# Kernel optimization log

Hardware: AMD Instinct MI355X
Metric: run time of the kernel (lower is better)

The kernel has to match this reference:

```python
import jax, jax.numpy as jnp
import numpy as np


def setup_inputs() -> dict:
    key = jax.random.key(0)
    ks = jax.random.split(key, 5)
    T, H, I, E = 8192, 2048, 1408, 16
    return {
        "x": jax.random.normal(ks[0], (T, H), dtype=jnp.float32),
        "gate_w": jax.random.normal(ks[1], (E, H), dtype=jnp.float32) * 0.02,
        "W1": jax.random.normal(ks[2], (E, I, H), dtype=jnp.float32) * 0.02,
        "Up": jax.random.normal(ks[3], (E, I, H), dtype=jnp.float32) * 0.02,
        "W2": jax.random.normal(ks[4], (E, H, I), dtype=jnp.float32) * 0.02,
        "topk": 2,
    }


def reference(x, gate_w, W1, Up, W2, topk):
    # x: [T, H]; gate_w: [E, H]; W1/Up: [E, I, H]; W2: [E, H, I]
    E = gate_w.shape[0]
    logits = x @ gate_w.T                                   # [T, E]
    topk_w, topk_ids = jax.lax.top_k(logits, topk)          # [T, K]
    topk_w = jax.nn.softmax(topk_w, axis=-1)                # softmax over selected experts
    # combine weight per (token, expert): sum of routing weights where expert selected
    cw = jnp.sum(jax.nn.one_hot(topk_ids, E, dtype=x.dtype) * topk_w[..., None], axis=1)  # [T, E]

    def body(acc, inputs):
        w1, up, w2, we = inputs                             # [I,H],[I,H],[H,I],[T]
        h = jax.nn.silu(x @ w1.T) * (x @ up.T)              # [T, I]
        return acc + we[:, None] * (h @ w2.T), None

    out, _ = jax.lax.scan(body, jnp.zeros_like(x), (W1, Up, W2, cw.T))
    return out
```

## Files before the change

kernel.cpp:

```cpp
#include <hip/hip_runtime.h>

static constexpr int kT = 8192;
static constexpr int kH = 2048;
static constexpr int kI = 1408;
static constexpr int kE = 16;

typedef __bf16 bf16x8 __attribute__((ext_vector_type(8)));
typedef float floatx4 __attribute__((ext_vector_type(4)));

__device__ __forceinline__ __bf16 f2bf(float f) { return (__bf16)f; }

__global__ void cvt_x_kernel(const float* __restrict__ x, __bf16* __restrict__ xb) {
    size_t i = ((size_t)blockIdx.x * 256 + threadIdx.x) * 8;
    float4 v0 = *(const float4*)(x + i);
    float4 v1 = *(const float4*)(x + i + 4);
    union { __bf16 b[8]; uint4 u; } o;
    o.b[0] = f2bf(v0.x); o.b[1] = f2bf(v0.y); o.b[2] = f2bf(v0.z); o.b[3] = f2bf(v0.w);
    o.b[4] = f2bf(v1.x); o.b[5] = f2bf(v1.y); o.b[6] = f2bf(v1.z); o.b[7] = f2bf(v1.w);
    *(uint4*)(xb + i) = o.u;
}

__global__ __launch_bounds__(256)
void gate_kernel(const float* __restrict__ x, const float* __restrict__ gw,
                 int* __restrict__ t_ids, float* __restrict__ t_w,
                 int* __restrict__ counts) {
    const int lane = threadIdx.x & 63;
    const int t = blockIdx.x * 4 + (threadIdx.x >> 6);
    float acc[kE];
#pragma unroll
    for (int e = 0; e < kE; ++e) acc[e] = 0.f;
    const float* xr = x + (size_t)t * kH;
    for (int h = lane; h < kH; h += 64) {
        const float xv = xr[h];
#pragma unroll
        for (int e = 0; e < kE; ++e) acc[e] += xv * gw[e * kH + h];
    }
#pragma unroll
    for (int e = 0; e < kE; ++e) {
        float v = acc[e];
        for (int off = 32; off > 0; off >>= 1) v += __shfl_xor(v, off, 64);
        acc[e] = v;
    }
    if (lane == 0) {
        int i0 = 0; float l0 = acc[0];
#pragma unroll
        for (int e = 1; e < kE; ++e) if (acc[e] > l0) { l0 = acc[e]; i0 = e; }
        int i1 = -1; float l1 = -3.4e38f;
#pragma unroll
        for (int e = 0; e < kE; ++e) if (e != i0 && acc[e] > l1) { l1 = acc[e]; i1 = e; }
        const float ex = __expf(l1 - l0);
        const float inv = 1.f / (1.f + ex);
        t_ids[2 * t] = i0; t_ids[2 * t + 1] = i1;
        t_w[2 * t] = inv;  t_w[2 * t + 1] = ex * inv;
        atomicAdd(counts + i0, 1);
        atomicAdd(counts + i1, 1);
    }
}

__global__ void scan_kernel(const int* __restrict__ counts, int* __restrict__ offs,
                            int* __restrict__ fill) {
    if (threadIdx.x == 0) {
        int s = 0;
        for (int e = 0; e < kE; ++e) { offs[e] = s; fill[e] = s; s += counts[e]; }
        offs[kE] = s;
    }
}

__global__ void scatter_kernel(const int* __restrict__ t_ids, const float* __restrict__ t_w,
                               int* __restrict__ fill, int* __restrict__ btok,
                               float* __restrict__ bw) {
    int t = blockIdx.x * 256 + threadIdx.x;
    if (t < kT) {
#pragma unroll
        for (int k = 0; k < 2; ++k) {
            int e = t_ids[2 * t + k];
            int pos = atomicAdd(fill + e, 1);
            btok[pos] = t;
            bw[pos] = t_w[2 * t + k];
        }
    }
}

__global__ __launch_bounds__(256, 2)
void gemm1_kernel(const __bf16* __restrict__ xb, const float* __restrict__ W1,
                  const float* __restrict__ Up, const int* __restrict__ btok,
                  const float* __restrict__ bw, const int* __restrict__ offs,
                  __bf16* __restrict__ hbuf) {
    const int e = blockIdx.z;
    const int seg0 = offs[e];
    const int ne = offs[e + 1] - seg0;
    const int m0 = blockIdx.y * 128;
    if (m0 >= ne) return;
    const int n0 = blockIdx.x * 64;

    __shared__ __align__(16) __bf16 sA[128 * 64];
    __shared__ __align__(16) __bf16 sB1[64 * 64];
    __shared__ __align__(16) __bf16 sB2[64 * 64];

    const int tid = threadIdx.x;

    const int ar = tid >> 3;
    const int ac = (tid & 7) * 8;
    const __bf16* aptr[4];
#pragma unroll
    for (int i = 0; i < 4; ++i) {
        int rr = m0 + ar + 32 * i;
        if (rr >= ne) rr = ne - 1;
        aptr[i] = xb + (size_t)btok[seg0 + rr] * kH + ac;
    }

    const int brr = tid >> 4;
    const int bcc = (tid & 15) * 4;
    const float* b1p = W1 + ((size_t)e * kI + n0 + brr) * kH + bcc;
    const float* b2p = Up + ((size_t)e * kI + n0 + brr) * kH + bcc;

    const int wid = tid >> 6, lane = tid & 63;
    const int wm = (wid >> 1) * 64, wn = (wid & 1) * 32;
    const int lr = lane & 15;
    const int lk = (lane >> 4) * 8;

    floatx4 acc1[4][2], acc2[4][2];
#pragma unroll
    for (int i = 0; i < 4; ++i)
#pragma unroll
        for (int j = 0; j < 2; ++j) { acc1[i][j] = (floatx4)0.f; acc2[i][j] = (floatx4)0.f; }

    for (int k0 = 0; k0 < kH; k0 += 64) {
        __syncthreads();
#pragma unroll
        for (int i = 0; i < 4; ++i) {
            uint4 v = *(const uint4*)(aptr[i] + k0);
            *(uint4*)(sA + (ar + 32 * i) * 64 + ac) = v;
        }
#pragma unroll
        for (int i = 0; i < 4; ++i) {
            float4 v1 = *(const float4*)(b1p + (size_t)(16 * i) * kH + k0);
            float4 v2 = *(const float4*)(b2p + (size_t)(16 * i) * kH + k0);
            union { __bf16 b[4]; uint2 u; } o1, o2;
            o1.b[0] = f2bf(v1.x); o1.b[1] = f2bf(v1.y); o1.b[2] = f2bf(v1.z); o1.b[3] = f2bf(v1.w);
            o2.b[0] = f2bf(v2.x); o2.b[1] = f2bf(v2.y); o2.b[2] = f2bf(v2.z); o2.b[3] = f2bf(v2.w);
            *(uint2*)(sB1 + (brr + 16 * i) * 64 + bcc) = o1.u;
            *(uint2*)(sB2 + (brr + 16 * i) * 64 + bcc) = o2.u;
        }
        __syncthreads();
#pragma unroll
        for (int ks = 0; ks < 2; ++ks) {
            const int kk = ks * 32 + lk;
            bf16x8 af[4], bf1[2], bf2[2];
#pragma unroll
            for (int i = 0; i < 4; ++i)
                af[i] = *(const bf16x8*)(sA + (wm + i * 16 + lr) * 64 + kk);
#pragma unroll
            for (int j = 0; j < 2; ++j) {
                bf1[j] = *(const bf16x8*)(sB1 + (wn + j * 16 + lr) * 64 + kk);
                bf2[j] = *(const bf16x8*)(sB2 + (wn + j * 16 + lr) * 64 + kk);
            }
#pragma unroll
            for (int i = 0; i < 4; ++i)
#pragma unroll
                for (int j = 0; j < 2; ++j) {
                    acc1[i][j] = __builtin_amdgcn_mfma_f32_16x16x32_bf16(af[i], bf1[j], acc1[i][j], 0, 0, 0);
                    acc2[i][j] = __builtin_amdgcn_mfma_f32_16x16x32_bf16(af[i], bf2[j], acc2[i][j], 0, 0, 0);
                }
        }
    }

    const int q4 = (lane >> 4) * 4;
#pragma unroll
    for (int i = 0; i < 4; ++i) {
#pragma unroll
        for (int r = 0; r < 4; ++r) {
            const int row = wm + i * 16 + q4 + r;
            if (m0 + row < ne) {
                const float wrt = bw[seg0 + m0 + row];
                __bf16* hp = hbuf + (size_t)(seg0 + m0 + row) * kI + n0 + wn + (lane & 15);
#pragma unroll
                for (int j = 0; j < 2; ++j) {
                    float a = acc1[i][j][r];
                    float b = acc2[i][j][r];
                    float s = a / (1.f + __expf(-a));
                    hp[j * 16] = f2bf(s * b * wrt);
                }
            }
        }
    }
}

__global__ __launch_bounds__(256, 2)
void gemm2_kernel(const __bf16* __restrict__ hbuf, const float* __restrict__ W2,
                  const int* __restrict__ btok, const int* __restrict__ offs,
                  float* __restrict__ out) {
    const int e = blockIdx.z;
    const int seg0 = offs[e];
    const int ne = offs[e + 1] - seg0;
    const int m0 = blockIdx.y * 128;
    if (m0 >= ne) return;
    const int n0 = blockIdx.x * 64;

    __shared__ __align__(16) __bf16 sA[128 * 64];
    __shared__ __align__(16) __bf16 sB[64 * 64];

    const int tid = threadIdx.x;
    const int ar = tid >> 3;
    const int ac = (tid & 7) * 8;
    const __bf16* aptr[4];
#pragma unroll
    for (int i = 0; i < 4; ++i) {
        int rr = m0 + ar + 32 * i;
        if (rr >= ne) rr = ne - 1;
        aptr[i] = hbuf + (size_t)(seg0 + rr) * kI + ac;
    }

    const int brr = tid >> 4;
    const int bcc = (tid & 15) * 4;
    const float* bp = W2 + ((size_t)e * kH + n0 + brr) * kI + bcc;

    const int wid = tid >> 6, lane = tid & 63;
    const int wm = (wid >> 1) * 64, wn = (wid & 1) * 32;
    const int lr = lane & 15;
    const int lk = (lane >> 4) * 8;

    floatx4 acc[4][2];
#pragma unroll
    for (int i = 0; i < 4; ++i)
#pragma unroll
        for (int j = 0; j < 2; ++j) acc[i][j] = (floatx4)0.f;

    for (int k0 = 0; k0 < kI; k0 += 64) {
        __syncthreads();
#pragma unroll
        for (int i = 0; i < 4; ++i) {
            uint4 v = *(const uint4*)(aptr[i] + k0);
            *(uint4*)(sA + (ar + 32 * i) * 64 + ac) = v;
        }
#pragma unroll
        for (int i = 0; i < 4; ++i) {
            float4 v1 = *(const float4*)(bp + (size_t)(16 * i) * kI + k0);
            union { __bf16 b[4]; uint2 u; } o1;
            o1.b[0] = f2bf(v1.x); o1.b[1] = f2bf(v1.y); o1.b[2] = f2bf(v1.z); o1.b[3] = f2bf(v1.w);
            *(uint2*)(sB + (brr + 16 * i) * 64 + bcc) = o1.u;
        }
        __syncthreads();
#pragma unroll
        for (int ks = 0; ks < 2; ++ks) {
            const int kk = ks * 32 + lk;
            bf16x8 af[4], bfr[2];
#pragma unroll
            for (int i = 0; i < 4; ++i)
                af[i] = *(const bf16x8*)(sA + (wm + i * 16 + lr) * 64 + kk);
#pragma unroll
            for (int j = 0; j < 2; ++j)
                bfr[j] = *(const bf16x8*)(sB + (wn + j * 16 + lr) * 64 + kk);
#pragma unroll
            for (int i = 0; i < 4; ++i)
#pragma unroll
                for (int j = 0; j < 2; ++j)
                    acc[i][j] = __builtin_amdgcn_mfma_f32_16x16x32_bf16(af[i], bfr[j], acc[i][j], 0, 0, 0);
        }
    }

    const int q4 = (lane >> 4) * 4;
#pragma unroll
    for (int i = 0; i < 4; ++i) {
#pragma unroll
        for (int r = 0; r < 4; ++r) {
            const int row = wm + i * 16 + q4 + r;
            if (m0 + row < ne) {
                const int tok = btok[seg0 + m0 + row];
                float* op = out + (size_t)tok * kH + n0 + wn + (lane & 15);
#pragma unroll
                for (int j = 0; j < 2; ++j)
                    atomicAdd(op + j * 16, acc[i][j][r]);
            }
        }
    }
}

extern "C" void kernel_launch(void* const* d_in, const int* in_sizes, int n_in,
                              void* d_out, int out_size, void* d_ws, size_t ws_size,
                              hipStream_t stream) {
    const float* x  = (const float*)d_in[0];
    const float* gw = (const float*)d_in[1];
    const float* W1 = (const float*)d_in[2];
    const float* Up = (const float*)d_in[3];
    const float* W2 = (const float*)d_in[4];
    float* out = (float*)d_out;

    char* ws = (char*)d_ws;
    size_t o = 0;
    __bf16* xb   = (__bf16*)(ws + o); o += (size_t)kT * kH * 2;
    __bf16* hbuf = (__bf16*)(ws + o); o += (size_t)(2 * kT) * kI * 2;
    int*   t_ids = (int*)(ws + o);    o += (size_t)(2 * kT) * 4;
    float* t_w   = (float*)(ws + o);  o += (size_t)(2 * kT) * 4;
    int*   btok  = (int*)(ws + o);    o += (size_t)(2 * kT) * 4;
    float* bw    = (float*)(ws + o);  o += (size_t)(2 * kT) * 4;
    int*   counts = (int*)(ws + o);   o += 64;
    int*   offs   = (int*)(ws + o);   o += 128;
    int*   fill   = (int*)(ws + o);   o += 64;

    hipMemsetAsync(out, 0, (size_t)kT * kH * sizeof(float), stream);
    hipMemsetAsync(counts, 0, kE * sizeof(int), stream);

    cvt_x_kernel<<<(kT * kH / 8) / 256, 256, 0, stream>>>(x, xb);
    gate_kernel<<<kT / 4, 256, 0, stream>>>(x, gw, t_ids, t_w, counts);
    scan_kernel<<<1, 64, 0, stream>>>(counts, offs, fill);
    scatter_kernel<<<(kT + 255) / 256, 256, 0, stream>>>(t_ids, t_w, fill, btok, bw);

    dim3 g1(kI / 64, 64, kE);
    gemm1_kernel<<<g1, 256, 0, stream>>>(xb, W1, Up, btok, bw, offs, hbuf);
    dim3 g2(kH / 64, 64, kE);
    gemm2_kernel<<<g2, 256, 0, stream>>>(hbuf, W2, btok, offs, out);
}
```

Baseline: 1.644 ms.

## Double-buffer LDS tiles with register prefetch and XOR swizzle in both GEMMs

```diff
diff --git a/kernel.cpp b/kernel.cpp
--- a/kernel.cpp
+++ b/kernel.cpp
@@ -10,14 +10,18 @@
 
 __device__ __forceinline__ __bf16 f2bf(float f) { return (__bf16)f; }
 
+__device__ __forceinline__ uint4 pack8(float4 a, float4 b) {
+    union { __bf16 h[8]; uint4 u; } o;
+    o.h[0] = f2bf(a.x); o.h[1] = f2bf(a.y); o.h[2] = f2bf(a.z); o.h[3] = f2bf(a.w);
+    o.h[4] = f2bf(b.x); o.h[5] = f2bf(b.y); o.h[6] = f2bf(b.z); o.h[7] = f2bf(b.w);
+    return o.u;
+}
+
 __global__ void cvt_x_kernel(const float* __restrict__ x, __bf16* __restrict__ xb) {
     size_t i = ((size_t)blockIdx.x * 256 + threadIdx.x) * 8;
     float4 v0 = *(const float4*)(x + i);
     float4 v1 = *(const float4*)(x + i + 4);
-    union { __bf16 b[8]; uint4 u; } o;
-    o.b[0] = f2bf(v0.x); o.b[1] = f2bf(v0.y); o.b[2] = f2bf(v0.z); o.b[3] = f2bf(v0.w);
-    o.b[4] = f2bf(v1.x); o.b[5] = f2bf(v1.y); o.b[6] = f2bf(v1.z); o.b[7] = f2bf(v1.w);
-    *(uint4*)(xb + i) = o.u;
+    *(uint4*)(xb + i) = pack8(v0, v1);
 }
 
 __global__ __launch_bounds__(256)
@@ -93,31 +97,39 @@
     if (m0 >= ne) return;
     const int n0 = blockIdx.x * 64;
 
-    __shared__ __align__(16) __bf16 sA[128 * 64];
-    __shared__ __align__(16) __bf16 sB1[64 * 64];
-    __shared__ __align__(16) __bf16 sB2[64 * 64];
+    __shared__ __align__(16) __bf16 sA[2][128 * 64];
+    __shared__ __align__(16) __bf16 sB1[2][64 * 64];
+    __shared__ __align__(16) __bf16 sB2[2][64 * 64];
 
     const int tid = threadIdx.x;
 
     const int ar = tid >> 3;
-    const int ac = (tid & 7) * 8;
-    const __bf16* aptr[4];
+    const int as = tid & 7;
+    const __bf16* aSrc[4];
+    int awoff[4];
 #pragma unroll
     for (int i = 0; i < 4; ++i) {
-        int rr = m0 + ar + 32 * i;
+        const int row = ar + 32 * i;
+        int rr = m0 + row;
         if (rr >= ne) rr = ne - 1;
-        aptr[i] = xb + (size_t)btok[seg0 + rr] * kH + ac;
-    }
-
-    const int brr = tid >> 4;
-    const int bcc = (tid & 15) * 4;
-    const float* b1p = W1 + ((size_t)e * kI + n0 + brr) * kH + bcc;
-    const float* b2p = Up + ((size_t)e * kI + n0 + brr) * kH + bcc;
+        aSrc[i] = xb + (size_t)btok[seg0 + rr] * kH + as * 8;
+        awoff[i] = row * 64 + ((as ^ (row & 7)) << 3);
+    }
+
+    const int bcf = as * 8;
+    const float* b1p = W1 + ((size_t)e * kI + n0 + ar) * kH + bcf;
+    const float* b2p = Up + ((size_t)e * kI + n0 + ar) * kH + bcf;
+    int bwoff[2];
+#pragma unroll
+    for (int i = 0; i < 2; ++i) {
+        const int row = ar + 32 * i;
+        bwoff[i] = row * 64 + ((as ^ (row & 7)) << 3);
+    }
 
     const int wid = tid >> 6, lane = tid & 63;
     const int wm = (wid >> 1) * 64, wn = (wid & 1) * 32;
     const int lr = lane & 15;
-    const int lk = (lane >> 4) * 8;
+    const int lkq = lane >> 4;
 
     floatx4 acc1[4][2], acc2[4][2];
 #pragma unroll
@@ -125,44 +137,77 @@
 #pragma unroll
         for (int j = 0; j < 2; ++j) { acc1[i][j] = (floatx4)0.f; acc2[i][j] = (floatx4)0.f; }
 
-    for (int k0 = 0; k0 < kH; k0 += 64) {
+    {
+        uint4 apf[4];
+#pragma unroll
+        for (int i = 0; i < 4; ++i) apf[i] = *(const uint4*)(aSrc[i]);
+#pragma unroll
+        for (int i = 0; i < 4; ++i) *(uint4*)(&sA[0][awoff[i]]) = apf[i];
+#pragma unroll
+        for (int i = 0; i < 2; ++i) {
+            float4 v0 = *(const float4*)(b1p + (size_t)(32 * i) * kH);
+            float4 v1 = *(const float4*)(b1p + (size_t)(32 * i) * kH + 4);
+            float4 v2 = *(const float4*)(b2p + (size_t)(32 * i) * kH);
+            float4 v3 = *(const float4*)(b2p + (size_t)(32 * i) * kH + 4);
+            *(uint4*)(&sB1[0][bwoff[i]]) = pack8(v0, v1);
+            *(uint4*)(&sB2[0][bwoff[i]]) = pack8(v2, v3);
+        }
+    }
+    __syncthreads();
+
+    int cb = 0;
+    constexpr int nK = kH / 64;
+    for (int t = 0; t < nK; ++t) {
+        const int nb = cb ^ 1;
+        const bool hn = (t + 1) < nK;
+        uint4 apf[4];
+        float4 p0[2], p1[2], p2[2], p3[2];
+        if (hn) {
+            const int kn = (t + 1) * 64;
+#pragma unroll
+            for (int i = 0; i < 4; ++i) apf[i] = *(const uint4*)(aSrc[i] + kn);
+#pragma unroll
+            for (int i = 0; i < 2; ++i) {
+                p0[i] = *(const float4*)(b1p + (size_t)(32 * i) * kH + kn);
+                p1[i] = *(const float4*)(b1p + (size_t)(32 * i) * kH + kn + 4);
+                p2[i] = *(const float4*)(b2p + (size_t)(32 * i) * kH + kn);
+                p3[i] = *(const float4*)(b2p + (size_t)(32 * i) * kH + kn + 4);
+            }
+        }
+#pragma unroll
+        for (int ks = 0; ks < 2; ++ks) {
+            bf16x8 af[4], bq1[2], bq2[2];
+#pragma unroll
+            for (int i = 0; i < 4; ++i) {
+                const int row = wm + i * 16 + lr;
+                af[i] = *(const bf16x8*)(&sA[cb][row * 64 + (((ks * 4 + lkq) ^ (row & 7)) << 3)]);
+            }
+#pragma unroll
+            for (int j = 0; j < 2; ++j) {
+                const int row = wn + j * 16 + lr;
+                const int so = row * 64 + (((ks * 4 + lkq) ^ (row & 7)) << 3);
+                bq1[j] = *(const bf16x8*)(&sB1[cb][so]);
+                bq2[j] = *(const bf16x8*)(&sB2[cb][so]);
+            }
+#pragma unroll
+            for (int i = 0; i < 4; ++i)
+#pragma unroll
+                for (int j = 0; j < 2; ++j) {
+                    acc1[i][j] = __builtin_amdgcn_mfma_f32_16x16x32_bf16(af[i], bq1[j], acc1[i][j], 0, 0, 0);
+                    acc2[i][j] = __builtin_amdgcn_mfma_f32_16x16x32_bf16(af[i], bq2[j], acc2[i][j], 0, 0, 0);
+                }
+        }
+        if (hn) {
+#pragma unroll
+            for (int i = 0; i < 4; ++i) *(uint4*)(&sA[nb][awoff[i]]) = apf[i];
+#pragma unroll
+            for (int i = 0; i < 2; ++i) {
+                *(uint4*)(&sB1[nb][bwoff[i]]) = pack8(p0[i], p1[i]);
+                *(uint4*)(&sB2[nb][bwoff[i]]) = pack8(p2[i], p3[i]);
+            }
+        }
         __syncthreads();
-#pragma unroll
-        for (int i = 0; i < 4; ++i) {
-            uint4 v = *(const uint4*)(aptr[i] + k0);
-            *(uint4*)(sA + (ar + 32 * i) * 64 + ac) = v;
-        }
-#pragma unroll
-        for (int i = 0; i < 4; ++i) {
-            float4 v1 = *(const float4*)(b1p + (size_t)(16 * i) * kH + k0);
-            float4 v2 = *(const float4*)(b2p + (size_t)(16 * i) * kH + k0);
-            union { __bf16 b[4]; uint2 u; } o1, o2;
-            o1.b[0] = f2bf(v1.x); o1.b[1] = f2bf(v1.y); o1.b[2] = f2bf(v1.z); o1.b[3] = f2bf(v1.w);
-            o2.b[0] = f2bf(v2.x); o2.b[1] = f2bf(v2.y); o2.b[2] = f2bf(v2.z); o2.b[3] = f2bf(v2.w);
-            *(uint2*)(sB1 + (brr + 16 * i) * 64 + bcc) = o1.u;
-            *(uint2*)(sB2 + (brr + 16 * i) * 64 + bcc) = o2.u;
-        }
-        __syncthreads();
-#pragma unroll
-        for (int ks = 0; ks < 2; ++ks) {
-            const int kk = ks * 32 + lk;
-            bf16x8 af[4], bf1[2], bf2[2];
-#pragma unroll
-            for (int i = 0; i < 4; ++i)
-                af[i] = *(const bf16x8*)(sA + (wm + i * 16 + lr) * 64 + kk);
-#pragma unroll
-            for (int j = 0; j < 2; ++j) {
-                bf1[j] = *(const bf16x8*)(sB1 + (wn + j * 16 + lr) * 64 + kk);
-                bf2[j] = *(const bf16x8*)(sB2 + (wn + j * 16 + lr) * 64 + kk);
-            }
-#pragma unroll
-            for (int i = 0; i < 4; ++i)
-#pragma unroll
-                for (int j = 0; j < 2; ++j) {
-                    acc1[i][j] = __builtin_amdgcn_mfma_f32_16x16x32_bf16(af[i], bf1[j], acc1[i][j], 0, 0, 0);
-                    acc2[i][j] = __builtin_amdgcn_mfma_f32_16x16x32_bf16(af[i], bf2[j], acc2[i][j], 0, 0, 0);
-                }
-        }
+        cb = nb;
     }
 
     const int q4 = (lane >> 4) * 4;
@@ -197,28 +242,37 @@
     if (m0 >= ne) return;
     const int n0 = blockIdx.x * 64;
 
-    __shared__ __align__(16) __bf16 sA[128 * 64];
-    __shared__ __align__(16) __bf16 sB[64 * 64];
+    __shared__ __align__(16) __bf16 sA[2][128 * 64];
+    __shared__ __align__(16) __bf16 sB[2][64 * 64];
 
     const int tid = threadIdx.x;
     const int ar = tid >> 3;
-    const int ac = (tid & 7) * 8;
-    const __bf16* aptr[4];
+    const int as = tid & 7;
+
+    const __bf16* aSrc[4];
+    int awoff[4];
 #pragma unroll
     for (int i = 0; i < 4; ++i) {
-        int rr = m0 + ar + 32 * i;
+        const int row = ar + 32 * i;
+        int rr = m0 + row;
         if (rr >= ne) rr = ne - 1;
-        aptr[i] = hbuf + (size_t)(seg0 + rr) * kI + ac;
-    }
-
-    const int brr = tid >> 4;
-    const int bcc = (tid & 15) * 4;
-    const float* bp = W2 + ((size_t)e * kH + n0 + brr) * kI + bcc;
+        aSrc[i] = hbuf + (size_t)(seg0 + rr) * kI + as * 8;
+        awoff[i] = row * 64 + ((as ^ (row & 7)) << 3);
+    }
+
+    const int bcf = as * 8;
+    const float* bp = W2 + ((size_t)e * kH + n0 + ar) * kI + bcf;
+    int bwoff[2];
+#pragma unroll
+    for (int i = 0; i < 2; ++i) {
+        const int row = ar + 32 * i;
+        bwoff[i] = row * 64 + ((as ^ (row & 7)) << 3);
+    }
 
     const int wid = tid >> 6, lane = tid & 63;
     const int wm = (wid >> 1) * 64, wn = (wid & 1) * 32;
     const int lr = lane & 15;
-    const int lk = (lane >> 4) * 8;
+    const int lkq = lane >> 4;
 
     floatx4 acc[4][2];
 #pragma unroll
@@ -226,37 +280,66 @@
 #pragma unroll
         for (int j = 0; j < 2; ++j) acc[i][j] = (floatx4)0.f;
 
-    for (int k0 = 0; k0 < kI; k0 += 64) {
+    {
+        uint4 apf[4];
+#pragma unroll
+        for (int i = 0; i < 4; ++i) apf[i] = *(const uint4*)(aSrc[i]);
+#pragma unroll
+        for (int i = 0; i < 4; ++i) *(uint4*)(&sA[0][awoff[i]]) = apf[i];
+#pragma unroll
+        for (int i = 0; i < 2; ++i) {
+            float4 v0 = *(const float4*)(bp + (size_t)(32 * i) * kI);
+            float4 v1 = *(const float4*)(bp + (size_t)(32 * i) * kI + 4);
+            *(uint4*)(&sB[0][bwoff[i]]) = pack8(v0, v1);
+        }
+    }
+    __syncthreads();
+
+    int cb = 0;
+    constexpr int nK = kI / 64;
+    for (int t = 0; t < nK; ++t) {
+        const int nb = cb ^ 1;
+        const bool hn = (t + 1) < nK;
+        uint4 apf[4];
+        float4 p0[2], p1[2];
+        if (hn) {
+            const int kn = (t + 1) * 64;
+#pragma unroll
+            for (int i = 0; i < 4; ++i) apf[i] = *(const uint4*)(aSrc[i] + kn);
+#pragma unroll
+            for (int i = 0; i < 2; ++i) {
+                p0[i] = *(const float4*)(bp + (size_t)(32 * i) * kI + kn);
+                p1[i] = *(const float4*)(bp + (size_t)(32 * i) * kI + kn + 4);
+            }
+        }
+#pragma unroll
+        for (int ks = 0; ks < 2; ++ks) {
+            bf16x8 af[4], bq[2];
+#pragma unroll
+            for (int i = 0; i < 4; ++i) {
+                const int row = wm + i * 16 + lr;
+                af[i] = *(const bf16x8*)(&sA[cb][row * 64 + (((ks * 4 + lkq) ^ (row & 7)) << 3)]);
+            }
+#pragma unroll
+            for (int j = 0; j < 2; ++j) {
+                const int row = wn + j * 16 + lr;
+                bq[j] = *(const bf16x8*)(&sB[cb][row * 64 + (((ks * 4 + lkq) ^ (row & 7)) << 3)]);
+            }
+#pragma unroll
+            for (int i = 0; i < 4; ++i)
+#pragma unroll
+                for (int j = 0; j < 2; ++j)
+                    acc[i][j] = __builtin_amdgcn_mfma_f32_16x16x32_bf16(af[i], bq[j], acc[i][j], 0, 0, 0);
+        }
+        if (hn) {
+#pragma unroll
+            for (int i = 0; i < 4; ++i) *(uint4*)(&sA[nb][awoff[i]]) = apf[i];
+#pragma unroll
+            for (int i = 0; i < 2; ++i)
+                *(uint4*)(&sB[nb][bwoff[i]]) = pack8(p0[i], p1[i]);
+        }
         __syncthreads();
-#pragma unroll
-        for (int i = 0; i < 4; ++i) {
-            uint4 v = *(const uint4*)(aptr[i] + k0);
-            *(uint4*)(sA + (ar + 32 * i) * 64 + ac) = v;
-        }
-#pragma unroll
-        for (int i = 0; i < 4; ++i) {
-            float4 v1 = *(const float4*)(bp + (size_t)(16 * i) * kI + k0);
-            union { __bf16 b[4]; uint2 u; } o1;
-            o1.b[0] = f2bf(v1.x); o1.b[1] = f2bf(v1.y); o1.b[2] = f2bf(v1.z); o1.b[3] = f2bf(v1.w);
-            *(uint2*)(sB + (brr + 16 * i) * 64 + bcc) = o1.u;
-        }
-        __syncthreads();
-#pragma unroll
-        for (int ks = 0; ks < 2; ++ks) {
-            const int kk = ks * 32 + lk;
-            bf16x8 af[4], bfr[2];
-#pragma unroll
-            for (int i = 0; i < 4; ++i)
-                af[i] = *(const bf16x8*)(sA + (wm + i * 16 + lr) * 64 + kk);
-#pragma unroll
-            for (int j = 0; j < 2; ++j)
-                bfr[j] = *(const bf16x8*)(sB + (wn + j * 16 + lr) * 64 + kk);
-#pragma unroll
-            for (int i = 0; i < 4; ++i)
-#pragma unroll
-                for (int j = 0; j < 2; ++j)
-                    acc[i][j] = __builtin_amdgcn_mfma_f32_16x16x32_bf16(af[i], bfr[j], acc[i][j], 0, 0, 0);
-        }
+        cb = nb;
     }
 
     const int q4 = (lane >> 4) * 4;
```

New measurement: 1.366 ms. 1.2x faster.
